# Kernel tuning notes

Hardware: AMD Instinct MI355X
Metric: run time of the kernel (lower is better)

Reference implementation:

```python
import jax, jax.numpy as jnp
import numpy as np
from jax import lax

B, H, W = 64, 40, 40
K = 24        # num_capsules == num_templates
TS = 11       # template_size
F = 16        # num_feature_maps
PI = 3.141592653589793


def setup_inputs() -> dict:
    key = jax.random.key(0)
    ks = jax.random.split(key, 12)
    def nrm(k, shape, s):
        return jax.random.normal(k, shape, dtype=jnp.float32) * s
    inp = {"x": jax.random.normal(ks[0], (B, 1, H, W), dtype=jnp.float32)}
    wshapes = [(K, 128, 1, 3, 3), (K, 128, 128, 3, 3), (K, 128, 128, 3, 3), (K, 128, 128, 3, 3), (K, F, 128, 1, 1)]
    for i, sh in enumerate(wshapes):
        fan_in = sh[2] * sh[3] * sh[4]
        inp["w%d" % (i + 1)] = nrm(ks[1 + i], sh, (2.0 / fan_in) ** 0.5)
        inp["b%d" % (i + 1)] = nrm(ks[6 + i], (K, sh[1]), 0.1)
    inp["templates"] = jax.random.normal(ks[11], (K, TS, TS), dtype=jnp.float32)
    return inp


def _capsule(x, w1, b1, w2, b2, w3, b3, w4, b4, w5, b5):
    # one part-capsule conv stack; x: [B,1,H,W]
    def cv(h, w, b, s):
        y = lax.conv_general_dilated(h, w, (s, s), 'VALID', dimension_numbers=('NCHW', 'OIHW', 'NCHW'))
        return y + b[None, :, None, None]
    h = jax.nn.relu(cv(x, w1, b1, 2))
    h = jax.nn.relu(cv(h, w2, b2, 2))
    h = jax.nn.relu(cv(h, w3, b3, 1))
    h = jax.nn.relu(cv(h, w4, b4, 1))
    return cv(h, w5, b5, 1)  # [B,F,5,5]


def _warp(templates, pose, Ho, Wo):
    # Batched replacement for the per-sample PIL affine + resize round-trip.
    # templates: [T,TS,TS]; pose: [B,T,6] = (angle_deg, tx, ty, scale, shear_x_deg, shear_y_deg)
    T_ = templates.shape[0]
    ang = jnp.deg2rad(pose[..., 0])
    tx, ty = pose[..., 1], pose[..., 2]
    sc = jnp.maximum(pose[..., 3], 1e-2)  # guard against scale==0 from ReLU
    shx = jnp.deg2rad(pose[..., 4])
    shy = jnp.deg2rad(pose[..., 5])
    cx = cy = (TS - 1) * 0.5
    # torchvision _get_inverse_affine_matrix
    a = jnp.cos(ang - shy) / jnp.cos(shy)
    b = -jnp.cos(ang - shy) * jnp.tan(shx) / jnp.cos(shy) - jnp.sin(ang)
    c = jnp.sin(ang - shy) / jnp.cos(shy)
    d = -jnp.sin(ang - shy) * jnp.tan(shx) / jnp.cos(shy) + jnp.cos(ang)
    m0 = d / sc; m1 = -b / sc; m3 = -c / sc; m4 = a / sc
    m2 = m0 * (-cx - tx) + m1 * (-cy - ty) + cx
    m5 = m3 * (-cx - tx) + m4 * (-cy - ty) + cy
    # output grid in template pixel coords (fuses the bilinear resize TS->HoxWo)
    gy = (jnp.arange(Ho, dtype=jnp.float32) + 0.5) * TS / Ho - 0.5
    gx = (jnp.arange(Wo, dtype=jnp.float32) + 0.5) * TS / Wo - 0.5
    yo, xo = jnp.meshgrid(gy, gx, indexing='ij')  # [Ho,Wo]
    xin = m0[..., None, None] * xo + m1[..., None, None] * yo + m2[..., None, None]  # [B,T,Ho,Wo]
    yin = m3[..., None, None] * xo + m4[..., None, None] * yo + m5[..., None, None]
    x0 = jnp.floor(xin); y0 = jnp.floor(yin)
    wx = xin - x0; wy = yin - y0
    x0i = x0.astype(jnp.int32); y0i = y0.astype(jnp.int32)
    tidx = jnp.arange(T_)[None, :, None, None]
    def tap(yi, xi):
        valid = (xi >= 0) & (xi < TS) & (yi >= 0) & (yi < TS)
        v = templates[tidx, jnp.clip(yi, 0, TS - 1), jnp.clip(xi, 0, TS - 1)]
        return jnp.where(valid, v, 0.0)
    return (tap(y0i, x0i) * (1 - wx) * (1 - wy) + tap(y0i, x0i + 1) * wx * (1 - wy)
            + tap(y0i + 1, x0i) * (1 - wx) * wy + tap(y0i + 1, x0i + 1) * wx * wy)


def reference(x, w1, b1, w2, b2, w3, b3, w4, b4, w5, b5, templates):
    out = jax.vmap(_capsule, in_axes=(None,) + (0,) * 10)(x, w1, b1, w2, b2, w3, b3, w4, b4, w5, b5)  # [K,B,F,5,5]
    # torch Softmax(2) on [B,Hc,Wc] attention map = softmax over each row (last axis)
    att = jax.nn.softmax(out[:, :, -1], axis=-1)                       # [K,B,5,5]
    pooled = jnp.sum(out[:, :, :-1] * att[:, :, None], axis=(-2, -1))  # [K,B,F-1]
    p = pooled.transpose(1, 0, 2)                                      # [B,K,F-1]
    x_m = jax.nn.relu(p[:, :, :6])
    d_m = jax.nn.sigmoid(p[:, :, 6:7])
    c_z = jax.nn.relu(p[:, :, 7:])
    Bn = x.shape[0]
    # PIL round-trip in the original detaches gradients from templates/poses
    tt = lax.stop_gradient(_warp(templates, x_m, H, W))                # [B,K,H,W]
    mix = jax.nn.softmax(d_m * tt.reshape(Bn, K, -1), axis=-1).reshape(Bn, K, H, W)
    std = jnp.std(x.reshape(Bn, -1), axis=-1, ddof=1).reshape(Bn, 1, 1, 1)
    mult = 1.0 / jnp.sqrt(std * 2.0 * PI)
    pw = -1.0 / (2.0 * std * std)
    g = mult * jnp.exp((lax.stop_gradient(x) - tt) ** 2 * pw)          # [B,K,H,W]
    ll = jnp.mean(jnp.sum(jnp.log(jnp.sum(g * mix, axis=1)), axis=(-2, -1)))
    tflat = jnp.broadcast_to(lax.stop_gradient(templates).reshape(1, K, TS * TS), (Bn, K, TS * TS))
    input_ocae = jnp.concatenate([lax.stop_gradient(d_m), lax.stop_gradient(x_m), tflat, c_z], axis=-1)
    return ll, input_ocae, lax.stop_gradient(x_m), lax.stop_gradient(d_m)
```

## Files before the change

### kernel.cpp

```cpp
#include <hip/hip_runtime.h>
#include <math.h>

#define TPB 256

typedef __attribute__((ext_vector_type(8))) short s16x8;
typedef __attribute__((ext_vector_type(4))) short s16x4;
typedef __attribute__((ext_vector_type(4))) float f32x4;
typedef unsigned int u32;

constexpr int Bn = 64, Kc = 24, TSz = 11;
constexpr int NBK = Bn * Kc;

constexpr size_t SZW_B    = (size_t)Kc * 36 * 4096 * 2;
constexpr size_t OFFB_W2  = 0;
constexpr size_t OFFB_W3  = OFFB_W2 + SZW_B;
constexpr size_t OFFB_W4  = OFFB_W3 + SZW_B;
constexpr size_t OFFB_DMV = OFFB_W4 + SZW_B;
constexpr size_t OFFB_TT  = OFFB_DMV + (size_t)NBK * 4;
constexpr size_t OFFB_ST  = OFFB_TT + (size_t)NBK * 1600 * 4;
constexpr size_t OFFB_MXS = OFFB_ST + 512;
constexpr size_t OFFB_PART= OFFB_MXS + (size_t)NBK * 2 * 4;

constexpr int OUT_OC = 1;
constexpr int OUT_XM = 1 + NBK * 136;
constexpr int OUT_DM = OUT_XM + NBK * 6;

__device__ __forceinline__ ushort f2b(float f) {
    union { float f; unsigned u; } c; c.f = f;
    unsigned r = c.u + 0x7fffu + ((c.u >> 16) & 1u);
    return (ushort)(r >> 16);
}
__device__ __forceinline__ float b2f(ushort h) {
    union { unsigned u; float f; } c; c.u = ((unsigned)h) << 16; return c.f;
}

__device__ __forceinline__ float blockReduceSum(float v) {
    __shared__ float red[4];
    __syncthreads();
#pragma unroll
    for (int o = 32; o > 0; o >>= 1) v += __shfl_down(v, o, 64);
    int lane = threadIdx.x & 63, wv = threadIdx.x >> 6;
    if (lane == 0) red[wv] = v;
    __syncthreads();
    return red[0] + red[1] + red[2] + red[3];
}

__device__ __forceinline__ float blockReduceMax(float v) {
    __shared__ float redm[4];
    __syncthreads();
#pragma unroll
    for (int o = 32; o > 0; o >>= 1) v = fmaxf(v, __shfl_down(v, o, 64));
    int lane = threadIdx.x & 63, wv = threadIdx.x >> 6;
    if (lane == 0) redm[wv] = v;
    __syncthreads();
    return fmaxf(fmaxf(redm[0], redm[1]), fmaxf(redm[2], redm[3]));
}

__global__ __launch_bounds__(TPB) void prep_k(
    const float* __restrict__ w2, const float* __restrict__ w3,
    const float* __restrict__ w4, const float* __restrict__ x,
    ushort* __restrict__ wt2, ushort* __restrict__ wt3,
    ushort* __restrict__ wt4, float* __restrict__ st) {
    const int bid = blockIdx.x;
    if (bid < 9216) {
        __shared__ float ld[1152];
        const float* w = bid < 3072 ? w2 : (bid < 6144 ? w3 : w4);
        ushort* wt = bid < 3072 ? wt2 : (bid < 6144 ? wt3 : wt4);
        const int kk = (bid % 3072) >> 7, cout = bid & 127;
        const float* src = w + (size_t)(kk * 128 + cout) * 1152;
        for (int i = threadIdx.x; i < 1152; i += TPB) ld[i] = src[i];
        __syncthreads();
        const int n = cout >> 4, l16 = cout & 15;
        for (int e = threadIdx.x; e < 1152; e += TPB) {
            int cb = e / 288, r = e - cb * 288, tap = r >> 5, c32 = r & 31;
            int cin = cb * 32 + c32;
            size_t d = (size_t)((kk * 4 + cb) * 9 + tap) * 4096
                     + n * 512 + (c32 >> 3) * 128 + l16 * 8 + (c32 & 7);
            wt[d] = f2b(ld[cin * 9 + tap]);
        }
    } else {
        const int b = bid - 9216;
        const float* xb = x + b * 1600;
        float s = 0.f, s2 = 0.f;
        for (int p = threadIdx.x; p < 1600; p += TPB) {
            float v = xb[p];
            s += v; s2 += v * v;
        }
        s = blockReduceSum(s);
        s2 = blockReduceSum(s2);
        if (threadIdx.x == 0) {
            float mean = s / 1600.f;
            float var = (s2 - 1600.f * mean * mean) / 1599.f;
            float sd = sqrtf(var);
            st[b * 2] = rsqrtf(sd * 6.283185307179586f);
            st[b * 2 + 1] = -1.f / (2.f * sd * sd);
        }
    }
}

__global__ __launch_bounds__(256) void convall_k(
    const float* __restrict__ x, const float* __restrict__ w1,
    const float* __restrict__ b1,
    const ushort* __restrict__ wt2, const float* __restrict__ b2,
    const ushort* __restrict__ wt3, const float* __restrict__ b3,
    const ushort* __restrict__ wt4, const float* __restrict__ b4,
    const float* __restrict__ w5, const float* __restrict__ b5,
    const float* __restrict__ tpl,
    float* __restrict__ dmv, float* __restrict__ tt,
    float* __restrict__ mxs, float* __restrict__ out) {
    __shared__ __align__(16) ushort pool[17680];
    float*  xs  = (float*)pool;
    ushort* As  = pool + 3200;
    ushort* h2L = pool;
    ushort* h3L = pool + 11016;
    float*  h4s = (float*)pool;
    float*  outs= (float*)(pool + 6400);
    float*  atts= (float*)(pool + 7200);
    float*  pooled = (float*)(pool + 7264);
    float*  tp  = (float*)(pool + 7400);

    const int bi = blockIdx.x;
    const int xcd = bi & 7, jj = bi >> 3;
    const int k = xcd * 3 + jj % 3, b = jj / 3;
    const int bkL = b * 24 + k;
    const int tid = threadIdx.x;
    const int w = tid >> 6, l = tid & 63, l16 = l & 15, g = l >> 4;
    const int mgrp = w >> 1, ngrp = w & 1;

    {
        constexpr int OP = 81, STR = 40;
        const int sl = tid & 7, p0 = tid >> 3;
        const ushort* wb = wt2 + (size_t)k * 36 * 4096 + ngrp * 2048 + g * 128 + l16 * 8;
        const float* w1k = w1 + (size_t)k * 1152;
        const float* b1k = b1 + k * 128;

        for (int i = tid; i < 400; i += 256)
            ((f32x4*)xs)[i] = ((const f32x4*)(x + b * 1600))[i];

        s16x8 breg[2][4];
#pragma unroll
        for (int n = 0; n < 4; ++n) breg[0][n] = *(const s16x8*)(wb + n * 512);
#pragma unroll
        for (int n = 0; n < 4; ++n) breg[1][n] = *(const s16x8*)(wb + 4096 + n * 512);

        f32x4 acc[3][4];
#pragma unroll
        for (int m = 0; m < 3; ++m)
#pragma unroll
            for (int n = 0; n < 4; ++n) acc[m][n] = (f32x4)0.f;

        int ibase[3];
#pragma unroll
        for (int m = 0; m < 3; ++m) {
            int row = (mgrp * 3 + m) * 16 + l16;
            row = row < OP ? row : OP - 1;
            int oy = row / 9, ox = row - oy * 9;
            ibase[m] = oy * 38 + ox * 2;
        }

        auto conv1_slab = [&](int cb) {
            float wq[36], bq[4];
            const float* wsrc = w1k + (cb * 32 + sl * 4) * 9;
#pragma unroll
            for (int i2 = 0; i2 < 9; ++i2) ((f32x4*)wq)[i2] = ((const f32x4*)wsrc)[i2];
            *(f32x4*)bq = *(const f32x4*)(b1k + cb * 32 + sl * 4);
            for (int p = p0; p < 361; p += 32) {
                int py = p / 19, px = p - py * 19;
                const float* xb = xs + py * 80 + px * 2;
                float xt[9];
#pragma unroll
                for (int dy = 0; dy < 3; ++dy)
#pragma unroll
                    for (int dx = 0; dx < 3; ++dx) xt[dy * 3 + dx] = xb[dy * 40 + dx];
                s16x4 v;
#pragma unroll
                for (int j2 = 0; j2 < 4; ++j2) {
                    float s2 = bq[j2];
#pragma unroll
                    for (int t9 = 0; t9 < 9; ++t9) s2 += wq[j2 * 9 + t9] * xt[t9];
                    v[j2] = (short)f2b(fmaxf(s2, 0.f));
                }
                *(s16x4*)(As + p * STR + 8 * ((sl >> 1) ^ ((p >> 3) & 1)) + (sl & 1) * 4) = v;
            }
        };

        __syncthreads();
        conv1_slab(0);
        __syncthreads();

#pragma unroll
        for (int cb = 0; cb < 4; ++cb) {
#pragma unroll
            for (int tap = 0; tap < 9; ++tap) {
                const int it = cb * 9 + tap;
                if (it + 1 < 36) {
                    const ushort* src = wb + (size_t)(it + 1) * 4096;
#pragma unroll
                    for (int n = 0; n < 4; ++n)
                        breg[(it + 1) & 1][n] = *(const s16x8*)(src + n * 512);
                }
                const int ioff = (tap / 3) * 19 + (tap % 3);
                s16x8 a[3];
#pragma unroll
                for (int m = 0; m < 3; ++m) {
                    int ip = ibase[m] + ioff;
                    a[m] = *(const s16x8*)(As + ip * STR + 8 * (g ^ ((ip >> 3) & 1)));
                }
#pragma unroll
                for (int n = 0; n < 4; ++n)
#pragma unroll
                    for (int m = 0; m < 3; ++m)
                        acc[m][n] = __builtin_amdgcn_mfma_f32_16x16x32_bf16(a[m], breg[it & 1][n], acc[m][n], 0, 0, 0);
            }
            if (cb < 3) {
                __syncthreads();
                conv1_slab(cb + 1);
                __syncthreads();
            }
        }
        __syncthreads();
#pragma unroll
        for (int n = 0; n < 4; ++n) {
            int cout = (ngrp * 4 + n) * 16 + l16;
            float bv = b2[k * 128 + cout];
#pragma unroll
            for (int m = 0; m < 3; ++m)
#pragma unroll
                for (int r = 0; r < 4; ++r) {
                    int row = (mgrp * 3 + m) * 16 + g * 4 + r;
                    if (row < OP)
                        h2L[row * 136 + cout] = f2b(fmaxf(acc[m][n][r] + bv, 0.f));
                }
        }
    }
    __syncthreads();

    {
        constexpr int OP = 49;
        const ushort* wb = wt3 + (size_t)k * 36 * 4096 + ngrp * 2048 + g * 128 + l16 * 8;
        s16x8 breg[2][4];
#pragma unroll
        for (int n = 0; n < 4; ++n) breg[0][n] = *(const s16x8*)(wb + n * 512);
#pragma unroll
        for (int n = 0; n < 4; ++n) breg[1][n] = *(const s16x8*)(wb + 4096 + n * 512);

        f32x4 acc[2][4];
#pragma unroll
        for (int m = 0; m < 2; ++m)
#pragma unroll
            for (int n = 0; n < 4; ++n) acc[m][n] = (f32x4)0.f;

        int ibase[2];
#pragma unroll
        for (int m = 0; m < 2; ++m) {
            int row = (mgrp * 2 + m) * 16 + l16;
            row = row < OP ? row : OP - 1;
            int oy = row / 7, ox = row - oy * 7;
            ibase[m] = oy * 9 + ox;
        }
#pragma unroll
        for (int cb = 0; cb < 4; ++cb)
#pragma unroll
            for (int tap = 0; tap < 9; ++tap) {
                const int it = cb * 9 + tap;
                if (it + 1 < 36) {
                    const ushort* src = wb + (size_t)(it + 1) * 4096;
#pragma unroll
                    for (int n = 0; n < 4; ++n)
                        breg[(it + 1) & 1][n] = *(const s16x8*)(src + n * 512);
                }
                const int ioff = (tap / 3) * 9 + (tap % 3);
                s16x8 a[2];
#pragma unroll
                for (int m = 0; m < 2; ++m)
                    a[m] = *(const s16x8*)(h2L + (ibase[m] + ioff) * 136 + cb * 32 + g * 8);
#pragma unroll
                for (int n = 0; n < 4; ++n)
#pragma unroll
                    for (int m = 0; m < 2; ++m)
                        acc[m][n] = __builtin_amdgcn_mfma_f32_16x16x32_bf16(a[m], breg[it & 1][n], acc[m][n], 0, 0, 0);
            }
#pragma unroll
        for (int n = 0; n < 4; ++n) {
            int cout = (ngrp * 4 + n) * 16 + l16;
            float bv = b3[k * 128 + cout];
#pragma unroll
            for (int m = 0; m < 2; ++m)
#pragma unroll
                for (int r = 0; r < 4; ++r) {
                    int row = (mgrp * 2 + m) * 16 + g * 4 + r;
                    if (row < OP)
                        h3L[row * 136 + cout] = f2b(fmaxf(acc[m][n][r] + bv, 0.f));
                }
        }
    }
    __syncthreads();

    {
        constexpr int OP = 25;
        const ushort* wb = wt4 + (size_t)k * 36 * 4096 + ngrp * 2048 + g * 128 + l16 * 8;
        s16x8 breg[2][4];
#pragma unroll
        for (int n = 0; n < 4; ++n) breg[0][n] = *(const s16x8*)(wb + n * 512);
#pragma unroll
        for (int n = 0; n < 4; ++n) breg[1][n] = *(const s16x8*)(wb + 4096 + n * 512);

        f32x4 acc[4];
#pragma unroll
        for (int n = 0; n < 4; ++n) acc[n] = (f32x4)0.f;

        int ibase;
        {
            int row = mgrp * 16 + l16;
            row = row < OP ? row : OP - 1;
            int oy = row / 5, ox = row - oy * 5;
            ibase = oy * 7 + ox;
        }
#pragma unroll
        for (int cb = 0; cb < 4; ++cb)
#pragma unroll
            for (int tap = 0; tap < 9; ++tap) {
                const int it = cb * 9 + tap;
                if (it + 1 < 36) {
                    const ushort* src = wb + (size_t)(it + 1) * 4096;
#pragma unroll
                    for (int n = 0; n < 4; ++n)
                        breg[(it + 1) & 1][n] = *(const s16x8*)(src + n * 512);
                }
                const int ioff = (tap / 3) * 7 + (tap % 3);
                s16x8 a = *(const s16x8*)(h3L + (ibase + ioff) * 136 + cb * 32 + g * 8);
#pragma unroll
                for (int n = 0; n < 4; ++n)
                    acc[n] = __builtin_amdgcn_mfma_f32_16x16x32_bf16(a, breg[it & 1][n], acc[n], 0, 0, 0);
            }
#pragma unroll
        for (int n = 0; n < 4; ++n) {
            int cout = (ngrp * 4 + n) * 16 + l16;
            float bv = b4[k * 128 + cout];
#pragma unroll
            for (int r = 0; r < 4; ++r) {
                int row = mgrp * 16 + g * 4 + r;
                if (row < OP)
                    h4s[cout * 25 + row] = fmaxf(acc[n][r] + bv, 0.f);
            }
        }
    }
    __syncthreads();

    for (int t = tid; t < 400; t += 256) {
        int f = t / 25, pix = t - f * 25;
        const float* wp = w5 + (size_t)(k * 16 + f) * 128;
        float s = b5[k * 16 + f];
        for (int c = 0; c < 128; ++c) s += wp[c] * h4s[c * 25 + pix];
        outs[t] = s;
    }
    __syncthreads();
    if (tid < 25) {
        int y5 = tid / 5;
        const float* row = outs + 15 * 25 + y5 * 5;
        float mx = row[0];
#pragma unroll
        for (int j = 1; j < 5; ++j) mx = fmaxf(mx, row[j]);
        float ssum = 0.f;
#pragma unroll
        for (int j = 0; j < 5; ++j) ssum += expf(row[j] - mx);
        atts[tid] = expf(outs[15 * 25 + tid] - mx) / ssum;
    }
    __syncthreads();
    if (tid < 15) {
        float s = 0.f;
        const float* row = outs + tid * 25;
#pragma unroll
        for (int p = 0; p < 25; ++p) s += row[p] * atts[p];
        pooled[tid] = s;
    }
    __syncthreads();
    float* oc = out + OUT_OC + (size_t)bkL * 136;
    if (tid < 6) {
        float v = fmaxf(pooled[tid], 0.f);
        oc[1 + tid] = v;
        out[OUT_XM + bkL * 6 + tid] = v;
    } else if (tid == 6) {
        float d = 1.f / (1.f + expf(-pooled[6]));
        dmv[bkL] = d;
        oc[0] = d;
        out[OUT_DM + bkL] = d;
    } else if (tid >= 7 && tid < 15) {
        oc[128 + tid - 7] = fmaxf(pooled[tid], 0.f);
    }
    for (int t = tid; t < 121; t += 256) oc[7 + t] = tpl[k * 121 + t];

    for (int i = tid; i < 121; i += 256) tp[i] = tpl[k * 121 + i];
    {
        const float D2R = 0.017453292519943295f;
        float ang = fmaxf(pooled[0], 0.f) * D2R;
        float txp = fmaxf(pooled[1], 0.f), typ = fmaxf(pooled[2], 0.f);
        float sc  = fmaxf(fmaxf(pooled[3], 0.f), 1e-2f);
        float shx = fmaxf(pooled[4], 0.f) * D2R;
        float shy = fmaxf(pooled[5], 0.f) * D2R;
        float dm  = 1.f / (1.f + expf(-pooled[6]));
        float cams = cosf(ang - shy), sams = sinf(ang - shy);
        float cshy = cosf(shy), tshx = tanf(shx);
        float av = cams / cshy;
        float bv = -cams * tshx / cshy - sinf(ang);
        float cv = sams / cshy;
        float dv = -sams * tshx / cshy + cosf(ang);
        float m0 = dv / sc, m1 = -bv / sc, m3 = -cv / sc, m4 = av / sc;
        float m2 = m0 * (-5.f - txp) + m1 * (-5.f - typ) + 5.f;
        float m5 = m3 * (-5.f - txp) + m4 * (-5.f - typ) + 5.f;
        __syncthreads();
        float* to = tt + (size_t)bkL * 1600;
        float tvl[7];
#pragma unroll
        for (int r = 0; r < 7; ++r) {
            int p = tid + r * 256;
            float val = 0.f;
            if (p < 1600) {
                int i = p / 40, jx = p - (p / 40) * 40;
                float gx = (jx + 0.5f) * (11.f / 40.f) - 0.5f;
                float gy = (i + 0.5f) * (11.f / 40.f) - 0.5f;
                float xin = m0 * gx + m1 * gy + m2;
                float yin = m3 * gx + m4 * gy + m5;
                float x0 = floorf(xin), y0 = floorf(yin);
                float wx = xin - x0, wy = yin - y0;
                int x0i = (int)x0, y0i = (int)y0;
                auto tapf = [&](int yy, int xx) -> float {
                    bool valid = (xx >= 0) && (xx < TSz) && (yy >= 0) && (yy < TSz);
                    int yc = min(max(yy, 0), TSz - 1), xc = min(max(xx, 0), TSz - 1);
                    float v = tp[yc * TSz + xc];
                    return valid ? v : 0.f;
                };
                float v00 = tapf(y0i, x0i),     v01 = tapf(y0i, x0i + 1);
                float v10 = tapf(y0i + 1, x0i), v11 = tapf(y0i + 1, x0i + 1);
                val = v00 * (1.f - wx) * (1.f - wy) + v01 * wx * (1.f - wy) +
                      v10 * (1.f - wx) * wy + v11 * wx * wy;
                to[p] = val;
            }
            tvl[r] = val;
        }
        float mx = -1e30f;
#pragma unroll
        for (int r = 0; r < 7; ++r) {
            int p = tid + r * 256;
            if (p < 1600) mx = fmaxf(mx, dm * tvl[r]);
        }
        mx = blockReduceMax(mx);
        float s = 0.f;
#pragma unroll
        for (int r = 0; r < 7; ++r) {
            int p = tid + r * 256;
            if (p < 1600) s += expf(dm * tvl[r] - mx);
        }
        s = blockReduceSum(s);
        if (tid == 0) { mxs[bkL * 2] = mx; mxs[bkL * 2 + 1] = s; }
    }
}

__global__ __launch_bounds__(TPB) void ll_k(const float* __restrict__ x,
                                            const float* __restrict__ tt,
                                            const float* __restrict__ dmv,
                                            const float* __restrict__ mxs,
                                            const float* __restrict__ st,
                                            float* __restrict__ part) {
    const int b = blockIdx.x, sp = blockIdx.y;
    __shared__ float dms[24], mxh[24], sih[24];
    if (threadIdx.x < 24) {
        int bk = b * 24 + threadIdx.x;
        dms[threadIdx.x] = dmv[bk];
        mxh[threadIdx.x] = mxs[bk * 2];
        sih[threadIdx.x] = 1.f / mxs[bk * 2 + 1];
    }
    __syncthreads();
    const float mult = st[b * 2], pw = st[b * 2 + 1];
    const float* xb = x + b * 1600;
    const float* tb = tt + (size_t)b * 24 * 1600;
    float acc = 0.f;
    int p = sp * 200 + threadIdx.x;
    if (threadIdx.x < 200) {
        float xv = xb[p];
        float ssum = 0.f;
        for (int k = 0; k < 24; ++k) {
            float tv = tb[(size_t)k * 1600 + p];
            float dd = xv - tv;
            float g = mult * expf(dd * dd * pw);
            float mixv = expf(dms[k] * tv - mxh[k]) * sih[k];
            ssum += g * mixv;
        }
        acc = logf(ssum);
    }
    acc = blockReduceSum(acc);
    if (threadIdx.x == 0) part[b * 8 + sp] = acc;
}

__global__ void fin_k(const float* __restrict__ part, float* __restrict__ out) {
    float v = 0.f;
#pragma unroll
    for (int q = 0; q < 8; ++q) v += part[threadIdx.x * 8 + q];
#pragma unroll
    for (int o = 32; o > 0; o >>= 1) v += __shfl_down(v, o, 64);
    if (threadIdx.x == 0) out[0] = v * (1.f / 64.f);
}

extern "C" void kernel_launch(void* const* d_in, const int* in_sizes, int n_in,
                              void* d_out, int out_size, void* d_ws, size_t ws_size,
                              hipStream_t stream) {
    const float* x   = (const float*)d_in[0];
    const float* w1  = (const float*)d_in[1];
    const float* b1  = (const float*)d_in[2];
    const float* w2  = (const float*)d_in[3];
    const float* b2  = (const float*)d_in[4];
    const float* w3  = (const float*)d_in[5];
    const float* b3  = (const float*)d_in[6];
    const float* w4  = (const float*)d_in[7];
    const float* b4  = (const float*)d_in[8];
    const float* w5  = (const float*)d_in[9];
    const float* b5  = (const float*)d_in[10];
    const float* tpl = (const float*)d_in[11];
    float* out = (float*)d_out;
    char* W = (char*)d_ws;

    ushort* wt2 = (ushort*)(W + OFFB_W2);
    ushort* wt3 = (ushort*)(W + OFFB_W3);
    ushort* wt4 = (ushort*)(W + OFFB_W4);
    float*  dmv  = (float*)(W + OFFB_DMV);
    float*  ttb  = (float*)(W + OFFB_TT);
    float*  stv  = (float*)(W + OFFB_ST);
    float*  mxs  = (float*)(W + OFFB_MXS);
    float*  part = (float*)(W + OFFB_PART);

    prep_k<<<3 * 3072 + Bn, TPB, 0, stream>>>(w2, w3, w4, x, wt2, wt3, wt4, stv);
    convall_k<<<NBK, 256, 0, stream>>>(x, w1, b1, wt2, b2, wt3, b3, wt4, b4,
                                       w5, b5, tpl, dmv, ttb, mxs, out);
    ll_k<<<dim3(Bn, 8), TPB, 0, stream>>>(x, ttb, dmv, mxs, stv, part);
    fin_k<<<1, 64, 0, stream>>>(part, out);
}
```

Measured before the change: 204.6 us.

## Double convall_k block to 512 threads, splitting output channels across more waves

The fused conv kernel now runs 8 waves per block instead of 4. Each wave owns 2 of the 16-wide output-channel tiles instead of 4, which halves its accumulator and B-operand registers. The conv1 slab loop is unrolled over a fixed trip count. The layer-2 weight prefetch is restructured so the first tap of each input-channel slab loads after the slab is written. The aim is more latency hiding and more waves per CU at the cost of fewer MFMAs per wave and more barrier participants. Any unseen sections that assume 256 threads could break.

New measurement: 227.5 us. 1.11x slower.

```diff
diff --git a/kernel.cpp b/kernel.cpp
--- a/kernel.cpp
+++ b/kernel.cpp
@@ -45,15 +45,32 @@
     return red[0] + red[1] + red[2] + red[3];
 }
 
-__device__ __forceinline__ float blockReduceMax(float v) {
-    __shared__ float redm[4];
+__device__ __forceinline__ float blockReduceSum512(float v) {
+    __shared__ float red8[8];
+    __syncthreads();
+#pragma unroll
+    for (int o = 32; o > 0; o >>= 1) v += __shfl_down(v, o, 64);
+    int lane = threadIdx.x & 63, wv = threadIdx.x >> 6;
+    if (lane == 0) red8[wv] = v;
+    __syncthreads();
+    float s = 0.f;
+#pragma unroll
+    for (int i = 0; i < 8; ++i) s += red8[i];
+    return s;
+}
+
+__device__ __forceinline__ float blockReduceMax512(float v) {
+    __shared__ float redm8[8];
     __syncthreads();
 #pragma unroll
     for (int o = 32; o > 0; o >>= 1) v = fmaxf(v, __shfl_down(v, o, 64));
     int lane = threadIdx.x & 63, wv = threadIdx.x >> 6;
-    if (lane == 0) redm[wv] = v;
-    __syncthreads();
-    return fmaxf(fmaxf(redm[0], redm[1]), fmaxf(redm[2], redm[3]));
+    if (lane == 0) redm8[wv] = v;
+    __syncthreads();
+    float m = redm8[0];
+#pragma unroll
+    for (int i = 1; i < 8; ++i) m = fmaxf(m, redm8[i]);
+    return m;
 }
 
 __global__ __launch_bounds__(TPB) void prep_k(
@@ -98,7 +115,7 @@
     }
 }
 
-__global__ __launch_bounds__(256) void convall_k(
+__global__ __launch_bounds__(512) void convall_k(
     const float* __restrict__ x, const float* __restrict__ w1,
     const float* __restrict__ b1,
     const ushort* __restrict__ wt2, const float* __restrict__ b2,
@@ -125,29 +142,23 @@
     const int bkL = b * 24 + k;
     const int tid = threadIdx.x;
     const int w = tid >> 6, l = tid & 63, l16 = l & 15, g = l >> 4;
-    const int mgrp = w >> 1, ngrp = w & 1;
+    const int mgrp = w >> 2, ngrp = w & 3;
 
     {
         constexpr int OP = 81, STR = 40;
         const int sl = tid & 7, p0 = tid >> 3;
-        const ushort* wb = wt2 + (size_t)k * 36 * 4096 + ngrp * 2048 + g * 128 + l16 * 8;
+        const ushort* wb = wt2 + (size_t)k * 36 * 4096 + ngrp * 1024 + g * 128 + l16 * 8;
         const float* w1k = w1 + (size_t)k * 1152;
         const float* b1k = b1 + k * 128;
 
-        for (int i = tid; i < 400; i += 256)
+        for (int i = tid; i < 400; i += 512)
             ((f32x4*)xs)[i] = ((const f32x4*)(x + b * 1600))[i];
 
-        s16x8 breg[2][4];
-#pragma unroll
-        for (int n = 0; n < 4; ++n) breg[0][n] = *(const s16x8*)(wb + n * 512);
-#pragma unroll
-        for (int n = 0; n < 4; ++n) breg[1][n] = *(const s16x8*)(wb + 4096 + n * 512);
-
-        f32x4 acc[3][4];
+        f32x4 acc[3][2];
 #pragma unroll
         for (int m = 0; m < 3; ++m)
 #pragma unroll
-            for (int n = 0; n < 4; ++n) acc[m][n] = (f32x4)0.f;
+            for (int n = 0; n < 2; ++n) acc[m][n] = (f32x4)0.f;
 
         int ibase[3];
 #pragma unroll
@@ -164,28 +175,35 @@
 #pragma unroll
             for (int i2 = 0; i2 < 9; ++i2) ((f32x4*)wq)[i2] = ((const f32x4*)wsrc)[i2];
             *(f32x4*)bq = *(const f32x4*)(b1k + cb * 32 + sl * 4);
-            for (int p = p0; p < 361; p += 32) {
-                int py = p / 19, px = p - py * 19;
-                const float* xb = xs + py * 80 + px * 2;
-                float xt[9];
-#pragma unroll
-                for (int dy = 0; dy < 3; ++dy)
-#pragma unroll
-                    for (int dx = 0; dx < 3; ++dx) xt[dy * 3 + dx] = xb[dy * 40 + dx];
-                s16x4 v;
-#pragma unroll
-                for (int j2 = 0; j2 < 4; ++j2) {
-                    float s2 = bq[j2];
-#pragma unroll
-                    for (int t9 = 0; t9 < 9; ++t9) s2 += wq[j2 * 9 + t9] * xt[t9];
-                    v[j2] = (short)f2b(fmaxf(s2, 0.f));
-                }
-                *(s16x4*)(As + p * STR + 8 * ((sl >> 1) ^ ((p >> 3) & 1)) + (sl & 1) * 4) = v;
+#pragma unroll
+            for (int jp = 0; jp < 6; ++jp) {
+                int p = p0 + jp * 64;
+                if (p < 361) {
+                    int py = p / 19, px = p - py * 19;
+                    const float* xb = xs + py * 80 + px * 2;
+                    float xt[9];
+#pragma unroll
+                    for (int dy = 0; dy < 3; ++dy)
+#pragma unroll
+                        for (int dx = 0; dx < 3; ++dx) xt[dy * 3 + dx] = xb[dy * 40 + dx];
+                    s16x4 v;
+#pragma unroll
+                    for (int j2 = 0; j2 < 4; ++j2) {
+                        float s2 = bq[j2];
+#pragma unroll
+                        for (int t9 = 0; t9 < 9; ++t9) s2 += wq[j2 * 9 + t9] * xt[t9];
+                        v[j2] = (short)f2b(fmaxf(s2, 0.f));
+                    }
+                    *(s16x4*)(As + p * STR + 8 * ((sl >> 1) ^ ((p >> 3) & 1)) + (sl & 1) * 4) = v;
+                }
             }
         };
 
+        s16x8 breg[2][2];
         __syncthreads();
         conv1_slab(0);
+#pragma unroll
+        for (int n = 0; n < 2; ++n) breg[0][n] = *(const s16x8*)(wb + n * 512);
         __syncthreads();
 
 #pragma unroll
@@ -193,10 +211,10 @@
 #pragma unroll
             for (int tap = 0; tap < 9; ++tap) {
                 const int it = cb * 9 + tap;
-                if (it + 1 < 36) {
+                if (tap < 8) {
                     const ushort* src = wb + (size_t)(it + 1) * 4096;
 #pragma unroll
-                    for (int n = 0; n < 4; ++n)
+                    for (int n = 0; n < 2; ++n)
                         breg[(it + 1) & 1][n] = *(const s16x8*)(src + n * 512);
                 }
                 const int ioff = (tap / 3) * 19 + (tap % 3);
@@ -207,7 +225,7 @@
                     a[m] = *(const s16x8*)(As + ip * STR + 8 * (g ^ ((ip >> 3) & 1)));
                 }
 #pragma unroll
-                for (int n = 0; n < 4; ++n)
+                for (int n = 0; n < 2; ++n)
 #pragma unroll
                     for (int m = 0; m < 3; ++m)
                         acc[m][n] = __builtin_amdgcn_mfma_f32_16x16x32_bf16(a[m], breg[it & 1][n], acc[m][n], 0, 0, 0);
@@ -215,13 +233,17 @@
             if (cb < 3) {
                 __syncthreads();
                 conv1_slab(cb + 1);
+                const ushort* src = wb + (size_t)((cb + 1) * 9) * 4096;
+#pragma unroll
+                for (int n = 0; n < 2; ++n)
+                    breg[((cb + 1) * 9) & 1][n] = *(const s16x8*)(src + n * 512);
                 __syncthreads();
             }
         }
         __syncthreads();
 #pragma unroll
-        for (int n = 0; n < 4; ++n) {
-            int cout = (ngrp * 4 + n) * 16 + l16;
+        for (int n = 0; n < 2; ++n) {
+            int cout = (ngrp * 2 + n) * 16 + l16;
             float bv = b2[k * 128 + cout];
 #pragma unroll
             for (int m = 0; m < 3; ++m)
@@ -237,18 +259,18 @@
 
     {
         constexpr int OP = 49;
-        const ushort* wb = wt3 + (size_t)k * 36 * 4096 + ngrp * 2048 + g * 128 + l16 * 8;
-        s16x8 breg[2][4];
-#pragma unroll
-        for (int n = 0; n < 4; ++n) breg[0][n] = *(const s16x8*)(wb + n * 512);
-#pragma unroll
-        for (int n = 0; n < 4; ++n) breg[1][n] = *(const s16x8*)(wb + 4096 + n * 512);
-
-        f32x4 acc[2][4];
+        const ushort* wb = wt3 + (size_t)k * 36 * 4096 + ngrp * 1024 + g * 128 + l16 * 8;
+        s16x8 breg[2][2];
+#pragma unroll
+        for (int n = 0; n < 2; ++n) breg[0][n] = *(const s16x8*)(wb + n * 512);
+#pragma unroll
+        for (int n = 0; n < 2; ++n) breg[1][n] = *(const s16x8*)(wb + 4096 + n * 512);
+
+        f32x4 acc[2][2];
 #pragma unroll
         for (int m = 0; m < 2; ++m)
 #pragma unroll
-            for (int n = 0; n < 4; ++n) acc[m][n] = (f32x4)0.f;
+            for (int n = 0; n < 2; ++n) acc[m][n] = (f32x4)0.f;
 
         int ibase[2];
 #pragma unroll
@@ -266,7 +288,7 @@
                 if (it + 1 < 36) {
                     const ushort* src = wb + (size_t)(it + 1) * 4096;
 #pragma unroll
-                    for (int n = 0; n < 4; ++n)
+                    for (int n = 0; n < 2; ++n)
                         breg[(it + 1) & 1][n] = *(const s16x8*)(src + n * 512);
                 }
                 const int ioff = (tap / 3) * 9 + (tap % 3);
@@ -275,14 +297,14 @@
                 for (int m = 0; m < 2; ++m)
                     a[m] = *(const s16x8*)(h2L + (ibase[m] + ioff) * 136 + cb * 32 + g * 8);
 #pragma unroll
-                for (int n = 0; n < 4; ++n)
+                for (int n = 0; n < 2; ++n)
 #pragma unroll
                     for (int m = 0; m < 2; ++m)
                         acc[m][n] = __builtin_amdgcn_mfma_f32_16x16x32_bf16(a[m], breg[it & 1][n], acc[m][n], 0, 0, 0);
             }
 #pragma unroll
-        for (int n = 0; n < 4; ++n) {
-            int cout = (ngrp * 4 + n) * 16 + l16;
+        for (int n = 0; n < 2; ++n) {
+            int cout = (ngrp * 2 + n) * 16 + l16;
             float bv = b3[k * 128 + cout];
 #pragma unroll
             for (int m = 0; m < 2; ++m)
@@ -298,16 +320,16 @@
 
     {
         constexpr int OP = 25;
-        const ushort* wb = wt4 + (size_t)k * 36 * 4096 + ngrp * 2048 + g * 128 + l16 * 8;
-        s16x8 breg[2][4];
-#pragma unroll
-        for (int n = 0; n < 4; ++n) breg[0][n] = *(const s16x8*)(wb + n * 512);
-#pragma unroll
-        for (int n = 0; n < 4; ++n) breg[1][n] = *(const s16x8*)(wb + 4096 + n * 512);
-
-        f32x4 acc[4];
-#pragma unroll
-        for (int n = 0; n < 4; ++n) acc[n] = (f32x4)0.f;
+        const ushort* wb = wt4 + (size_t)k * 36 * 4096 + ngrp * 1024 + g * 128 + l16 * 8;
+        s16x8 breg[2][2];
+#pragma unroll
+        for (int n = 0; n < 2; ++n) breg[0][n] = *(const s16x8*)(wb + n * 512);
+#pragma unroll
+        for (int n = 0; n < 2; ++n) breg[1][n] = *(const s16x8*)(wb + 4096 + n * 512);
+
+        f32x4 acc[2];
+#pragma unroll
+        for (int n = 0; n < 2; ++n) acc[n] = (f32x4)0.f;
 
         int ibase;
         {
@@ -324,18 +346,18 @@
                 if (it + 1 < 36) {
                     const ushort* src = wb + (size_t)(it + 1) * 4096;
 #pragma unroll
-                    for (int n = 0; n < 4; ++n)
+                    for (int n = 0; n < 2; ++n)
                         breg[(it + 1) & 1][n] = *(const s16x8*)(src + n * 512);
                 }
                 const int ioff = (tap / 3) * 7 + (tap % 3);
                 s16x8 a = *(const s16x8*)(h3L + (ibase + ioff) * 136 + cb * 32 + g * 8);
 #pragma unroll
-                for (int n = 0; n < 4; ++n)
+                for (int n = 0; n < 2; ++n)
                     acc[n] = __builtin_amdgcn_mfma_f32_16x16x32_bf16(a, breg[it & 1][n], acc[n], 0, 0, 0);
             }
 #pragma unroll
-        for (int n = 0; n < 4; ++n) {
-            int cout = (ngrp * 4 + n) * 16 + l16;
+        for (int n = 0; n < 2; ++n) {
+            int cout = (ngrp * 2 + n) * 16 + l16;
             float bv = b4[k * 128 + cout];
 #pragma unroll
             for (int r = 0; r < 4; ++r) {
@@ -347,7 +369,7 @@
     }
     __syncthreads();
 
-    for (int t = tid; t < 400; t += 256) {
+    for (int t = tid; t < 400; t += 512) {
         int f = t / 25, pix = t - f * 25;
         const float* wp = w5 + (size_t)(k * 16 + f) * 128;
         float s = b5[k * 16 + f];
@@ -388,9 +410,9 @@
     } else if (tid >= 7 && tid < 15) {
         oc[128 + tid - 7] = fmaxf(pooled[tid], 0.f);
     }
-    for (int t = tid; t < 121; t += 256) oc[7 + t] = tpl[k * 121 + t];
-
-    for (int i = tid; i < 121; i += 256) tp[i] = tpl[k * 121 + i];
+    for (int t = tid; t < 121; t += 512) oc[7 + t] = tpl[k * 121 + t];
+
+    for (int i = tid; i < 121; i += 512) tp[i] = tpl[k * 121 + i];
     {
         const float D2R = 0.017453292519943295f;
         float ang = fmaxf(pooled[0], 0.f) * D2R;
@@ -410,10 +432,10 @@
         float m5 = m3 * (-5.f - txp) + m4 * (-5.f - typ) + 5.f;
         __syncthreads();
         float* to = tt + (size_t)bkL * 1600;
-        float tvl[7];
-#pragma unroll
-        for (int r = 0; r < 7; ++r) {
-            int p = tid + r * 256;
+        float tvl[4];
+#pragma unroll
+        for (int r = 0; r < 4; ++r) {
+            int p = tid + r * 512;
             float val = 0.f;
             if (p < 1600) {
                 int i = p / 40, jx = p - (p / 40) * 40;
@@ -440,18 +462,18 @@
         }
         float mx = -1e30f;
 #pragma unroll
-        for (int r = 0; r < 7; ++r) {
-            int p = tid + r * 256;
+        for (int r = 0; r < 4; ++r) {
+            int p = tid + r * 512;
             if (p < 1600) mx = fmaxf(mx, dm * tvl[r]);
         }
-        mx = blockReduceMax(mx);
+        mx = blockReduceMax512(mx);
         float s = 0.f;
 #pragma unroll
-        for (int r = 0; r < 7; ++r) {
-            int p = tid + r * 256;
+        for (int r = 0; r < 4; ++r) {
+            int p = tid + r * 512;
             if (p < 1600) s += expf(dm * tvl[r] - mx);
         }
-        s = blockReduceSum(s);
+        s = blockReduceSum512(s);
         if (tid == 0) { mxs[bkL * 2] = mx; mxs[bkL * 2 + 1] = s; }
     }
 }
@@ -529,7 +551,7 @@
     float*  part = (float*)(W + OFFB_PART);
 
     prep_k<<<3 * 3072 + Bn, TPB, 0, stream>>>(w2, w3, w4, x, wt2, wt3, wt4, stv);
-    convall_k<<<NBK, 256, 0, stream>>>(x, w1, b1, wt2, b2, wt3, b3, wt4, b4,
+    convall_k<<<NBK, 512, 0, stream>>>(x, w1, b1, wt2, b2, wt3, b3, wt4, b4,
                                        w5, b5, tpl, dmv, ttb, mxs, out);
     ll_k<<<dim3(Bn, 8), TPB, 0, stream>>>(x, ttb, dmv, mxs, stv, part);
     fin_k<<<1, 64, 0, stream>>>(part, out);
```
